# Kernel optimization log

Hardware: AMD Instinct MI355X
Metric: run time of the kernel (lower is better)

The kernel has to match this reference:

```python
import jax, jax.numpy as jnp
import numpy as np

N, D = 8192, 256
NEG_BIG = -9e15


def setup_inputs() -> dict:
    key = jax.random.key(0)
    k1, k2, k3 = jax.random.split(key, 3)
    h = jax.random.normal(k1, (N, D), dtype=jnp.float32)
    adj = jax.random.randint(k2, (N, N), 0, 2, dtype=jnp.int32)
    # xavier_uniform for a of shape (2D, 1): bound = sqrt(6/(2D+1))
    bound = np.sqrt(6.0 / (2 * D + 1)).astype(np.float32)
    a = jax.random.uniform(k3, (2 * D, 1), dtype=jnp.float32, minval=-bound, maxval=bound)
    return {"h": h, "adj": adj, "a": a}


def reference(h, adj, a):
    d = h.shape[1]
    h1 = h @ a[:d]            # [N, 1]
    h2 = h @ a[d:]            # [N, 1]
    e = jax.nn.leaky_relu(h1 + h2.T, negative_slope=0.01)  # [N, N]
    attention = jnp.where(adj > 0, e, NEG_BIG)
    attention = jax.nn.softmax(attention, axis=1)
    # dropout skipped: eval mode (training=False)
    return attention @ h      # [N, D]
```

## Files before the change

kernel.cpp:

```cpp
#include <hip/hip_runtime.h>
#include <hip/hip_bf16.h>

#define NTOT 8192
#define DDIM 256
#define RTILE 16
#define JSPL 2
#define JBLK (NTOT / JSPL)
#define JWAVE (JBLK / 2)
#define NITER (JWAVE / 32)
#define NTSTR 131584
#define HTF_ELEMS (16 * NTSTR)

typedef __attribute__((ext_vector_type(8))) short short8;
typedef __attribute__((ext_vector_type(4))) float floatx4;
typedef __attribute__((ext_vector_type(4))) int intx4;

static __device__ __forceinline__ short bfp(float f) {
  __hip_bfloat16 b = __float2bfloat16(f);
  return *(short*)&b;
}

__global__ __launch_bounds__(256) void gat_scores(const float* __restrict__ h,
                                                  const float* __restrict__ a,
                                                  float* __restrict__ s1,
                                                  float* __restrict__ s2) {
  int row  = blockIdx.x * 4 + (threadIdx.x >> 6);
  int lane = threadIdx.x & 63;
  const float* hr = h + (size_t)row * DDIM;
  float p1 = 0.f, p2 = 0.f;
#pragma unroll
  for (int k = 0; k < DDIM / 64; ++k) {
    int idx  = lane + 64 * k;
    float hv = hr[idx];
    p1 += hv * a[idx];
    p2 += hv * a[DDIM + idx];
  }
#pragma unroll
  for (int off = 32; off > 0; off >>= 1) {
    p1 += __shfl_down(p1, off, 64);
    p2 += __shfl_down(p2, off, 64);
  }
  if (lane == 0) { s1[row] = p1; s2[row] = p2; }
}

__global__ __launch_bounds__(256) void gat_hpack(const float* __restrict__ h,
                                                 ushort* __restrict__ hTf) {
  __shared__ float tile[64][257];
  const int t    = threadIdx.x;
  const int lane = t & 63;
  const int w    = t >> 6;
  const int quad = lane >> 4;
  const int c    = lane & 15;
  const int i0   = blockIdx.x * 64;

#pragma unroll
  for (int it = 0; it < 16; ++it) {
    int r = it * 4 + w;
    float4 v = *(const float4*)(h + (size_t)(i0 + r) * DDIM + lane * 4);
    tile[r][lane * 4 + 0] = v.x; tile[r][lane * 4 + 1] = v.y;
    tile[r][lane * 4 + 2] = v.z; tile[r][lane * 4 + 3] = v.w;
  }
  __syncthreads();

#pragma unroll
  for (int k = 0; k < 4; ++k) {
    const int n = 4 * k + w;
#pragma unroll
    for (int jbl = 0; jbl < 2; ++jbl) {
      short8 vv;
#pragma unroll
      for (int i = 0; i < 8; ++i) {
        float f = tile[jbl * 32 + quad * 8 + i][n * 16 + c];
        vv[i] = bfp(f);
      }
      *(short8*)(hTf + ((size_t)(n * 257 + i0 / 32 + jbl) * 64 + lane) * 8) = vv;
    }
  }
}

__global__ __launch_bounds__(256, 4) void gat_attn(const ushort* __restrict__ hTf,
                                                   const int* __restrict__ adj,
                                                   const float* __restrict__ s1,
                                                   const float* __restrict__ s2,
                                                   float* __restrict__ pout,
                                                   float* __restrict__ plp) {
  __shared__ float slab[2][32][64];
  __shared__ float lpred[2][16];

  const int t    = threadIdx.x;
  const int lane = t & 63;
  const int w    = t >> 6;
  const int quad = lane >> 4;
  const int c    = lane & 15;
  const int ch   = w & 1;
  const int jc   = w >> 1;
  const int r0   = blockIdx.x * RTILE;
  const int jb   = blockIdx.y;
  const int j0   = jb * JBLK + jc * JWAVE;

  const float a1 = s1[r0 + c];

  const int*    ap = adj + (size_t)(r0 + c) * NTOT + j0 + quad * 8;
  const float*  sp = s2 + j0 + quad * 8;
  const ushort* hb = hTf + (size_t)(ch * 8) * NTSTR + ((size_t)(j0 / 32) * 64 + lane) * 8;

  floatx4 acc[8];
#pragma unroll
  for (int q = 0; q < 8; ++q) acc[q] = (floatx4){0.f, 0.f, 0.f, 0.f};

  float lp = 0.f;
  short8 bA[4], bB[4];
  intx4  aj0, aj1;
  float4 sv0, sv1;

  #define LDA(jt)                                                              \
    {                                                                          \
      const int* p_ = ap + (size_t)(jt) * 32;                                  \
      aj0 = __builtin_nontemporal_load((const intx4*)p_);                      \
      aj1 = __builtin_nontemporal_load((const intx4*)(p_ + 4));                \
      sv0 = *(const float4*)(sp + (jt) * 32);                                  \
      sv1 = *(const float4*)(sp + (jt) * 32 + 4);                              \
    }
  #define LDBA(jt)                                                             \
    _Pragma("unroll")                                                          \
    for (int q = 0; q < 4; ++q)                                                \
      bA[q] = *(const short8*)(hb + (size_t)(jt) * 512 + (size_t)q * NTSTR);
  #define LDBB(jt)                                                             \
    _Pragma("unroll")                                                          \
    for (int q = 0; q < 4; ++q)                                                \
      bB[q] = *(const short8*)(hb + (size_t)(jt) * 512 + (size_t)(4 + q) * NTSTR);

  LDBA(0)
  LDBB(0)
  LDA(0)

  for (int jt = 0; jt < NITER; ++jt) {
    const int jn = (jt + 1) & (NITER - 1);

    const float sarr[8] = {sv0.x, sv0.y, sv0.z, sv0.w, sv1.x, sv1.y, sv1.z, sv1.w};
    const int   aarr[8] = {aj0[0], aj0[1], aj0[2], aj0[3], aj1[0], aj1[1], aj1[2], aj1[3]};
    short8 pa;
#pragma unroll
    for (int i = 0; i < 8; ++i) {
      const float e  = a1 + sarr[i];
      const float l  = fmaxf(e, 0.01f * e);
      const float pe = __expf(l);
      const float p  = (aarr[i] > 0) ? pe : 0.f;
      lp += p;
      pa[i] = bfp(p);
    }

    LDA(jn)

#pragma unroll
    for (int q = 0; q < 4; ++q)
      acc[q] = __builtin_amdgcn_mfma_f32_16x16x32_bf16(pa, bA[q], acc[q], 0, 0, 0);
    LDBA(jn)

#pragma unroll
    for (int q = 0; q < 4; ++q)
      acc[4 + q] = __builtin_amdgcn_mfma_f32_16x16x32_bf16(pa, bB[q], acc[4 + q], 0, 0, 0);
    LDBB(jn)
  }
  #undef LDA
  #undef LDBA
  #undef LDBB

  lp += __shfl_xor(lp, 16, 64);
  lp += __shfl_xor(lp, 32, 64);

  if (jc == 1) {
#pragma unroll
    for (int q = 0; q < 8; ++q)
#pragma unroll
      for (int r = 0; r < 4; ++r) slab[ch][q * 4 + r][lane] = acc[q][r];
    if (lane < 16) lpred[ch][lane] = lp;
  }
  __syncthreads();
  if (jc == 0) {
#pragma unroll
    for (int q = 0; q < 8; ++q)
#pragma unroll
      for (int r = 0; r < 4; ++r) acc[q][r] += slab[ch][q * 4 + r][lane];
    lp += lpred[ch][c];

    float* pob = pout + (size_t)jb * NTOT * DDIM;
#pragma unroll
    for (int q = 0; q < 8; ++q)
#pragma unroll
      for (int r = 0; r < 4; ++r)
        pob[(size_t)(r0 + quad * 4 + r) * DDIM + ch * 128 + q * 16 + c] = acc[q][r];
    if (ch == 0 && quad == 0) plp[(size_t)jb * NTOT + r0 + c] = lp;
  }
}

__global__ __launch_bounds__(256) void gat_combine(const float* __restrict__ pout,
                                                   const float* __restrict__ plp,
                                                   float* __restrict__ out) {
  const int idx = blockIdx.x * 256 + threadIdx.x;
  const int row = idx >> 6;
  float4 a = ((const float4*)pout)[idx];
  float4 b = ((const float4*)(pout + (size_t)NTOT * DDIM))[idx];
  float inv = 1.f / (plp[row] + plp[NTOT + row]);
  float4 r;
  r.x = (a.x + b.x) * inv;
  r.y = (a.y + b.y) * inv;
  r.z = (a.z + b.z) * inv;
  r.w = (a.w + b.w) * inv;
  __builtin_nontemporal_store(r.x, &((float*)out)[idx * 4 + 0]);
  __builtin_nontemporal_store(r.y, &((float*)out)[idx * 4 + 1]);
  __builtin_nontemporal_store(r.z, &((float*)out)[idx * 4 + 2]);
  __builtin_nontemporal_store(r.w, &((float*)out)[idx * 4 + 3]);
}

extern "C" void kernel_launch(void* const* d_in, const int* in_sizes, int n_in,
                              void* d_out, int out_size, void* d_ws, size_t ws_size,
                              hipStream_t stream) {
  const float* h   = (const float*)d_in[0];
  const int*   adj = (const int*)d_in[1];
  const float* a   = (const float*)d_in[2];
  float* out = (float*)d_out;

  float*    s1    = (float*)d_ws;
  float*    s2    = s1 + NTOT;
  ushort*   hTf   = (ushort*)(s2 + NTOT);
  float*    pout  = (float*)(hTf + HTF_ELEMS);
  float*    plp   = pout + (size_t)JSPL * NTOT * DDIM;

  gat_scores<<<NTOT / 4, 256, 0, stream>>>(h, a, s1, s2);
  gat_hpack<<<NTOT / 64, 256, 0, stream>>>(h, hTf);
  gat_attn<<<dim3(NTOT / RTILE, JSPL), 256, 0, stream>>>(hTf, adj, s1, s2, pout, plp);
  gat_combine<<<(NTOT * DDIM / 4) / 256, 256, 0, stream>>>(pout, plp, out);
}
```

Measured before the change: 520.9 us.

## Factor exp of leaky-relu into per-node tables and fuse split-K combine into attention

Since exp is monotonic, exp(leaky(a+b)) equals max(e^a·e^b, e^{0.01a}·e^{0.01b}). The scores kernel therefore precomputes these exponentials per node, and the inner loop replaces exp with two multiplies and a max. The attention kernel now uses 1024-thread blocks covering 32 rows and the full j range across 4 wave groups, reducing partials in shared memory and writing the normalized output directly. This removes the pout/plp workspace and the separate combine kernel. It adds sched_barriers and more LDS reductions and syncs, and the products can overflow for large scores because no max is subtracted.

Result: no change. 519.7 us (-0.2%).

```diff
diff --git a/kernel.cpp b/kernel.cpp
--- a/kernel.cpp
+++ b/kernel.cpp
@@ -3,10 +3,8 @@
 
 #define NTOT 8192
 #define DDIM 256
-#define RTILE 16
-#define JSPL 2
-#define JBLK (NTOT / JSPL)
-#define JWAVE (JBLK / 2)
+#define ROWS 32
+#define JWAVE 2048
 #define NITER (JWAVE / 32)
 #define NTSTR 131584
 #define HTF_ELEMS (16 * NTSTR)
@@ -22,8 +20,8 @@
 
 __global__ __launch_bounds__(256) void gat_scores(const float* __restrict__ h,
                                                   const float* __restrict__ a,
-                                                  float* __restrict__ s1,
-                                                  float* __restrict__ s2) {
+                                                  float2* __restrict__ rc,
+                                                  float2* __restrict__ etab) {
   int row  = blockIdx.x * 4 + (threadIdx.x >> 6);
   int lane = threadIdx.x & 63;
   const float* hr = h + (size_t)row * DDIM;
@@ -40,7 +38,10 @@
     p1 += __shfl_down(p1, off, 64);
     p2 += __shfl_down(p2, off, 64);
   }
-  if (lane == 0) { s1[row] = p1; s2[row] = p2; }
+  if (lane == 0) {
+    rc[row]   = make_float2(__expf(p1), __expf(0.01f * p1));
+    etab[row] = make_float2(__expf(p2), __expf(0.01f * p2));
+  }
 }
 
 __global__ __launch_bounds__(256) void gat_hpack(const float* __restrict__ h,
@@ -78,31 +79,32 @@
   }
 }
 
-__global__ __launch_bounds__(256, 4) void gat_attn(const ushort* __restrict__ hTf,
-                                                   const int* __restrict__ adj,
-                                                   const float* __restrict__ s1,
-                                                   const float* __restrict__ s2,
-                                                   float* __restrict__ pout,
-                                                   float* __restrict__ plp) {
-  __shared__ float slab[2][32][64];
-  __shared__ float lpred[2][16];
+__global__ __launch_bounds__(1024, 4) void gat_attn(const ushort* __restrict__ hTf,
+                                                    const int* __restrict__ adj,
+                                                    const float2* __restrict__ rc,
+                                                    const float2* __restrict__ etab,
+                                                    float* __restrict__ out) {
+  __shared__ float slab[8][32][64];
+  __shared__ float lsum[4][32];
 
   const int t    = threadIdx.x;
   const int lane = t & 63;
   const int w    = t >> 6;
   const int quad = lane >> 4;
   const int c    = lane & 15;
-  const int ch   = w & 1;
-  const int jc   = w >> 1;
-  const int r0   = blockIdx.x * RTILE;
-  const int jb   = blockIdx.y;
-  const int j0   = jb * JBLK + jc * JWAVE;
-
-  const float a1 = s1[r0 + c];
-
-  const int*    ap = adj + (size_t)(r0 + c) * NTOT + j0 + quad * 8;
-  const float*  sp = s2 + j0 + quad * 8;
-  const ushort* hb = hTf + (size_t)(ch * 8) * NTSTR + ((size_t)(j0 / 32) * 64 + lane) * 8;
+  const int rg   = w & 1;
+  const int cg   = (w >> 1) & 1;
+  const int jg   = w >> 2;
+  const int r0   = blockIdx.x * ROWS;
+  const int rb   = r0 + rg * 16;
+  const int j0   = jg * JWAVE;
+
+  const float2 rcv = rc[rb + c];
+  const float E1 = rcv.x, E2 = rcv.y;
+
+  const int*    ap  = adj + (size_t)(rb + c) * NTOT + j0 + quad * 8;
+  const float*  etb = (const float*)(etab + j0 + quad * 8);
+  const ushort* hb  = hTf + (size_t)(8 * cg) * NTSTR + (size_t)(j0 / 32) * 512 + lane * 8;
 
   floatx4 acc[8];
 #pragma unroll
@@ -111,15 +113,21 @@
   float lp = 0.f;
   short8 bA[4], bB[4];
   intx4  aj0, aj1;
-  float4 sv0, sv1;
+  float4 ea, eb, ec, ed;
 
   #define LDA(jt)                                                              \
     {                                                                          \
       const int* p_ = ap + (size_t)(jt) * 32;                                  \
       aj0 = __builtin_nontemporal_load((const intx4*)p_);                      \
       aj1 = __builtin_nontemporal_load((const intx4*)(p_ + 4));                \
-      sv0 = *(const float4*)(sp + (jt) * 32);                                  \
-      sv1 = *(const float4*)(sp + (jt) * 32 + 4);                              \
+    }
+  #define LDE(jt)                                                              \
+    {                                                                          \
+      const float* e_ = etb + (size_t)(jt) * 64;                               \
+      ea = ((const float4*)e_)[0];                                             \
+      eb = ((const float4*)e_)[1];                                             \
+      ec = ((const float4*)e_)[2];                                             \
+      ed = ((const float4*)e_)[3];                                             \
     }
   #define LDBA(jt)                                                             \
     _Pragma("unroll")                                                          \
@@ -133,84 +141,89 @@
   LDBA(0)
   LDBB(0)
   LDA(0)
+  LDE(0)
 
   for (int jt = 0; jt < NITER; ++jt) {
     const int jn = (jt + 1) & (NITER - 1);
 
-    const float sarr[8] = {sv0.x, sv0.y, sv0.z, sv0.w, sv1.x, sv1.y, sv1.z, sv1.w};
-    const int   aarr[8] = {aj0[0], aj0[1], aj0[2], aj0[3], aj1[0], aj1[1], aj1[2], aj1[3]};
+    const int   am[8] = {aj0[0], aj0[1], aj0[2], aj0[3], aj1[0], aj1[1], aj1[2], aj1[3]};
+    const float tp[16] = {ea.x, ea.y, ea.z, ea.w, eb.x, eb.y, eb.z, eb.w,
+                          ec.x, ec.y, ec.z, ec.w, ed.x, ed.y, ed.z, ed.w};
     short8 pa;
 #pragma unroll
     for (int i = 0; i < 8; ++i) {
-      const float e  = a1 + sarr[i];
-      const float l  = fmaxf(e, 0.01f * e);
-      const float pe = __expf(l);
-      const float p  = (aarr[i] > 0) ? pe : 0.f;
+      const float p = (am[i] > 0) ? fmaxf(E1 * tp[2 * i], E2 * tp[2 * i + 1]) : 0.f;
       lp += p;
       pa[i] = bfp(p);
     }
 
     LDA(jn)
+    LDE(jn)
+    __builtin_amdgcn_sched_barrier(0);
 
 #pragma unroll
     for (int q = 0; q < 4; ++q)
       acc[q] = __builtin_amdgcn_mfma_f32_16x16x32_bf16(pa, bA[q], acc[q], 0, 0, 0);
     LDBA(jn)
+    __builtin_amdgcn_sched_barrier(0);
 
 #pragma unroll
     for (int q = 0; q < 4; ++q)
       acc[4 + q] = __builtin_amdgcn_mfma_f32_16x16x32_bf16(pa, bB[q], acc[4 + q], 0, 0, 0);
     LDBB(jn)
+    __builtin_amdgcn_sched_barrier(0);
   }
   #undef LDA
+  #undef LDE
   #undef LDBA
   #undef LDBB
 
   lp += __shfl_xor(lp, 16, 64);
   lp += __shfl_xor(lp, 32, 64);
-
-  if (jc == 1) {
-#pragma unroll
-    for (int q = 0; q < 8; ++q)
-#pragma unroll
-      for (int r = 0; r < 4; ++r) slab[ch][q * 4 + r][lane] = acc[q][r];
-    if (lane < 16) lpred[ch][lane] = lp;
-  }
-  __syncthreads();
-  if (jc == 0) {
-#pragma unroll
-    for (int q = 0; q < 8; ++q)
-#pragma unroll
-      for (int r = 0; r < 4; ++r) acc[q][r] += slab[ch][q * 4 + r][lane];
-    lp += lpred[ch][c];
-
-    float* pob = pout + (size_t)jb * NTOT * DDIM;
+  if (cg == 0 && lane < 16) lsum[jg][rg * 16 + lane] = lp;
+
+  const int sidx = rg * 2 + cg;
+  if (jg >= 2) {
 #pragma unroll
     for (int q = 0; q < 8; ++q)
 #pragma unroll
       for (int r = 0; r < 4; ++r)
-        pob[(size_t)(r0 + quad * 4 + r) * DDIM + ch * 128 + q * 16 + c] = acc[q][r];
-    if (ch == 0 && quad == 0) plp[(size_t)jb * NTOT + r0 + c] = lp;
-  }
-}
-
-__global__ __launch_bounds__(256) void gat_combine(const float* __restrict__ pout,
-                                                   const float* __restrict__ plp,
-                                                   float* __restrict__ out) {
-  const int idx = blockIdx.x * 256 + threadIdx.x;
-  const int row = idx >> 6;
-  float4 a = ((const float4*)pout)[idx];
-  float4 b = ((const float4*)(pout + (size_t)NTOT * DDIM))[idx];
-  float inv = 1.f / (plp[row] + plp[NTOT + row]);
-  float4 r;
-  r.x = (a.x + b.x) * inv;
-  r.y = (a.y + b.y) * inv;
-  r.z = (a.z + b.z) * inv;
-  r.w = (a.w + b.w) * inv;
-  __builtin_nontemporal_store(r.x, &((float*)out)[idx * 4 + 0]);
-  __builtin_nontemporal_store(r.y, &((float*)out)[idx * 4 + 1]);
-  __builtin_nontemporal_store(r.z, &((float*)out)[idx * 4 + 2]);
-  __builtin_nontemporal_store(r.w, &((float*)out)[idx * 4 + 3]);
+        slab[(jg - 2) * 4 + sidx][q * 4 + r][lane] = acc[q][r];
+  }
+  __syncthreads();
+  if (jg < 2) {
+#pragma unroll
+    for (int q = 0; q < 8; ++q)
+#pragma unroll
+      for (int r = 0; r < 4; ++r)
+        acc[q][r] += slab[jg * 4 + sidx][q * 4 + r][lane];
+  }
+  __syncthreads();
+  if (jg == 1) {
+#pragma unroll
+    for (int q = 0; q < 8; ++q)
+#pragma unroll
+      for (int r = 0; r < 4; ++r)
+        slab[sidx][q * 4 + r][lane] = acc[q][r];
+  }
+  __syncthreads();
+  if (jg == 0) {
+    float linv[4];
+#pragma unroll
+    for (int r = 0; r < 4; ++r) {
+      const int lr = rg * 16 + quad * 4 + r;
+      linv[r] = 1.f / (lsum[0][lr] + lsum[1][lr] + lsum[2][lr] + lsum[3][lr]);
+    }
+#pragma unroll
+    for (int q = 0; q < 8; ++q)
+#pragma unroll
+      for (int r = 0; r < 4; ++r) {
+        float v = acc[q][r] + slab[sidx][q * 4 + r][lane];
+        __builtin_nontemporal_store(
+            v * linv[r],
+            &out[(size_t)(rb + quad * 4 + r) * DDIM + cg * 128 + q * 16 + c]);
+      }
+  }
 }
 
 extern "C" void kernel_launch(void* const* d_in, const int* in_sizes, int n_in,
@@ -221,14 +234,11 @@
   const float* a   = (const float*)d_in[2];
   float* out = (float*)d_out;
 
-  float*    s1    = (float*)d_ws;
-  float*    s2    = s1 + NTOT;
-  ushort*   hTf   = (ushort*)(s2 + NTOT);
-  float*    pout  = (float*)(hTf + HTF_ELEMS);
-  float*    plp   = pout + (size_t)JSPL * NTOT * DDIM;
-
-  gat_scores<<<NTOT / 4, 256, 0, stream>>>(h, a, s1, s2);
+  float2*   rc    = (float2*)d_ws;
+  float2*   etab  = rc + NTOT;
+  ushort*   hTf   = (ushort*)(etab + NTOT);
+
+  gat_scores<<<NTOT / 4, 256, 0, stream>>>(h, a, rc, etab);
   gat_hpack<<<NTOT / 64, 256, 0, stream>>>(h, hTf);
-  gat_attn<<<dim3(NTOT / RTILE, JSPL), 256, 0, stream>>>(hTf, adj, s1, s2, pout, plp);
-  gat_combine<<<(NTOT * DDIM / 4) / 256, 256, 0, stream>>>(pout, plp, out);
-}
+  gat_attn<<<NTOT / ROWS, 1024, 0, stream>>>(hTf, adj, rc, etab, out);
+}
```
